# Optimization experiments

Measured on AMD Instinct MI355X. Metric: run time of the kernel, lower is better.

## Reference

```python
import jax, jax.numpy as jnp
import numpy as np

EPS = 1e-16


def setup_inputs() -> dict:
    key = jax.random.key(0)
    ks = jax.random.split(key, 8)
    B, C, F, H = 524288, 10, 10, 8  # batch, clusters, feats/cluster, tail hidden
    HC = 8  # head hidden = ceil(10 * 0.75)
    return {
        "x": jax.random.uniform(ks[0], (B, C * F), dtype=jnp.float32),
        "tail_enc_w": jax.random.normal(ks[1], (C, H, F), dtype=jnp.float32) * 0.3,
        "tail_enc_b": jax.random.normal(ks[2], (C, H), dtype=jnp.float32) * 0.1,
        "tail_dec_w": jax.random.normal(ks[3], (C, F, H), dtype=jnp.float32) * 0.3,
        "tail_dec_b": jax.random.normal(ks[4], (C, F), dtype=jnp.float32) * 0.1,
        "tail_nmin": jnp.zeros((C, F), dtype=jnp.float32),
        "tail_nmax": jnp.ones((C, F), dtype=jnp.float32),
        "head_enc_w": jax.random.normal(ks[5], (HC, C), dtype=jnp.float32) * 0.3,
        "head_enc_b": jax.random.normal(ks[6], (HC,), dtype=jnp.float32) * 0.1,
        "head_dec_w": jax.random.normal(ks[7], (C, HC), dtype=jnp.float32) * 0.3,
        "head_dec_b": jnp.zeros((C,), dtype=jnp.float32),
        "head_nmin": jnp.zeros((C,), dtype=jnp.float32),
        "head_nmax": jnp.ones((C,), dtype=jnp.float32),
    }


def reference(x, tail_enc_w, tail_enc_b, tail_dec_w, tail_dec_b,
              tail_nmin, tail_nmax, head_enc_w, head_enc_b,
              head_dec_w, head_dec_b, head_nmin, head_nmax):
    B = x.shape[0]
    C, H, F = tail_enc_w.shape
    # split the 100 features into C contiguous clusters of size F: [B, C, F]
    xc = x.reshape(B, C, F)
    # per-tail min-max normalisation (BaseAutoencoder.normalise)
    xn = (xc - tail_nmin) / (tail_nmax - tail_nmin + EPS)
    # all tails batched into one grouped matmul (sigmoid(Linear) twice)
    h = jax.nn.sigmoid(jnp.einsum('bcf,chf->bch', xn, tail_enc_w) + tail_enc_b)
    rec = jax.nn.sigmoid(jnp.einsum('bch,cfh->bcf', h, tail_dec_w) + tail_dec_b)
    # RMSE per (packet, cluster); infer mode => no log
    loss = jnp.sqrt(jnp.mean((rec - xn) ** 2, axis=-1))  # [B, C]
    tails = jnp.where(loss == 0, jnp.float32(0.01), loss)
    # head-level min-max normalisation (Kitsune.normalise)
    t = (tails - head_nmin) / (head_nmax - head_nmin + EPS)
    hh = jax.nn.sigmoid(t @ head_enc_w.T + head_enc_b)
    x_hat = jax.nn.sigmoid(hh @ head_dec_w.T + head_dec_b)
    return x_hat, t
```

## Files before the change

kernel.cpp:

```cpp
#include <hip/hip_runtime.h>

#define KEPS  1e-16f
#define LOG2E 1.44269504088896340736f

typedef float v2f __attribute__((ext_vector_type(2)));


__global__ void kitsune_prep(
    const float* __restrict__ tew, const float* __restrict__ teb,
    const float* __restrict__ tdw, const float* __restrict__ tdb,
    const float* __restrict__ tnmin, const float* __restrict__ tnmax,
    const float* __restrict__ hew, const float* __restrict__ heb,
    const float* __restrict__ hdw, const float* __restrict__ hdb,
    const float* __restrict__ hnmin, const float* __restrict__ hnmax,
    float* __restrict__ ws)
{
    const int i = threadIdx.x;
    for (int k = i; k < 100; k += 256) {
        float s = 1.0f / (tnmax[k] - tnmin[k] + KEPS);
        ws[k]        = s;
        ws[100 + k]  = -tnmin[k] * s;
        ws[1880 + k] = tdb[k] * -LOG2E;
    }
    for (int k = i; k < 800; k += 256) {
        ws[200 + k]  = tew[k] * -LOG2E;
        ws[1080 + k] = tdw[k] * -LOG2E;
    }
    for (int k = i; k < 80; k += 256) {
        ws[1000 + k] = teb[k] * -LOG2E;
        ws[2000 + k] = hew[k] * -LOG2E;
        ws[2088 + k] = hdw[k] * -LOG2E;
    }
    if (i < 10) {
        float s = 1.0f / (hnmax[i] - hnmin[i] + KEPS);
        ws[1980 + i] = s;
        ws[1990 + i] = -hnmin[i] * s;
        ws[2168 + i] = hdb[i] * -LOG2E;
    }
    if (i < 8) ws[2080 + i] = heb[i] * -LOG2E;
}

__device__ __forceinline__ float sig2(float a) {
    return __builtin_amdgcn_rcpf(1.0f + __builtin_amdgcn_exp2f(a));
}

__global__ __launch_bounds__(320) void kitsune_fused(
    const float* __restrict__ x,
    const float* __restrict__ ws,
    float* __restrict__ out_xhat,
    float* __restrict__ out_t,
    int B)
{
    __shared__ float xs[64 * 102];
    __shared__ float ts[64 * 11];

    const int tid  = threadIdx.x;
    const int base = (int)blockIdx.x * 64;
    const int rows = min(64, B - base);
    const int n25  = rows * 25;

    {
        const float4* gx = reinterpret_cast<const float4*>(x) + (size_t)base * 25;
        #pragma unroll
        for (int n = 0; n < 5; ++n) {
            int idx = tid + n * 320;
            if (idx < n25) {
                float4 v = gx[idx];
                int row = idx / 25;
                int q   = idx - row * 25;
                float* d = xs + row * 102 + q * 4;
                *reinterpret_cast<float2*>(d)     = make_float2(v.x, v.y);
                *reinterpret_cast<float2*>(d + 2) = make_float2(v.z, v.w);
            }
        }
    }
    __syncthreads();

    const int r = tid & 63;

    #pragma unroll
    for (int k = 0; k < 2; ++k) {
        const int c = __builtin_amdgcn_readfirstlane((tid >> 6) + 5 * k);

        v2f xp[5];
        #pragma unroll
        for (int j = 0; j < 5; ++j)
            xp[j] = *reinterpret_cast<const v2f*>(xs + r * 102 + c * 10 + 2 * j);

        const v2f* sc2 = reinterpret_cast<const v2f*>(ws + c * 10);
        const v2f* bi2 = reinterpret_cast<const v2f*>(ws + 100 + c * 10);
        #pragma unroll
        for (int j = 0; j < 5; ++j)
            xp[j] = __builtin_elementwise_fma(xp[j], sc2[j], bi2[j]);

        v2f hv[4];
        #pragma unroll
        for (int i = 0; i < 8; ++i) {
            const v2f* w2 = reinterpret_cast<const v2f*>(ws + 200 + (c * 8 + i) * 10);
            v2f a2 = w2[0] * xp[0];
            #pragma unroll
            for (int j = 1; j < 5; ++j)
                a2 = __builtin_elementwise_fma(w2[j], xp[j], a2);
            hv[i >> 1][i & 1] = sig2(ws[1000 + c * 8 + i] + a2.x + a2.y);
        }

        v2f ss2 = {0.0f, 0.0f};
        float dprev = 0.0f;
        #pragma unroll
        for (int f = 0; f < 10; ++f) {
            const v2f* w2 = reinterpret_cast<const v2f*>(ws + 1080 + (c * 10 + f) * 8);
            v2f a2 = w2[0] * hv[0];
            #pragma unroll
            for (int i = 1; i < 4; ++i)
                a2 = __builtin_elementwise_fma(w2[i], hv[i], a2);
            float rec = sig2(ws[1880 + c * 10 + f] + a2.x + a2.y);
            float d   = rec - xp[f >> 1][f & 1];
            if (f & 1) {
                v2f d2 = {dprev, d};
                ss2 = __builtin_elementwise_fma(d2, d2, ss2);
            } else {
                dprev = d;
            }
        }
        float l    = __builtin_amdgcn_sqrtf((ss2.x + ss2.y) * 0.1f);
        float tail = (l == 0.0f) ? 0.01f : l;
        float tv   = fmaf(tail, ws[1980 + c], ws[1990 + c]);

        ts[r * 11 + c] = tv;
        if (r < rows)
            out_t[(size_t)(base + r) * 10 + c] = tv;
    }
    __syncthreads();

    if (tid < 64 && tid < rows) {
        const float* tr = ts + tid * 11;
        v2f tp[5];
        #pragma unroll
        for (int j = 0; j < 5; ++j)
            tp[j] = v2f{tr[2 * j], tr[2 * j + 1]};

        v2f hv[4];
        #pragma unroll
        for (int i = 0; i < 8; ++i) {
            const v2f* w2 = reinterpret_cast<const v2f*>(ws + 2000 + i * 10);
            v2f a2 = w2[0] * tp[0];
            #pragma unroll
            for (int j = 1; j < 5; ++j)
                a2 = __builtin_elementwise_fma(w2[j], tp[j], a2);
            hv[i >> 1][i & 1] = sig2(ws[2080 + i] + a2.x + a2.y);
        }

        float xh[10];
        #pragma unroll
        for (int c = 0; c < 10; ++c) {
            const v2f* w2 = reinterpret_cast<const v2f*>(ws + 2088 + c * 8);
            v2f a2 = w2[0] * hv[0];
            #pragma unroll
            for (int i = 1; i < 4; ++i)
                a2 = __builtin_elementwise_fma(w2[i], hv[i], a2);
            xh[c] = sig2(ws[2168 + c] + a2.x + a2.y);
        }

        float* po = out_xhat + (size_t)(base + tid) * 10;
        #pragma unroll
        for (int j = 0; j < 5; ++j)
            *reinterpret_cast<float2*>(po + 2 * j) = make_float2(xh[2 * j], xh[2 * j + 1]);
    }
}

extern "C" void kernel_launch(void* const* d_in, const int* in_sizes, int n_in,
                              void* d_out, int out_size, void* d_ws, size_t ws_size,
                              hipStream_t stream) {
    const float* x          = (const float*)d_in[0];
    const float* tail_enc_w = (const float*)d_in[1];
    const float* tail_enc_b = (const float*)d_in[2];
    const float* tail_dec_w = (const float*)d_in[3];
    const float* tail_dec_b = (const float*)d_in[4];
    const float* tail_nmin  = (const float*)d_in[5];
    const float* tail_nmax  = (const float*)d_in[6];
    const float* head_enc_w = (const float*)d_in[7];
    const float* head_enc_b = (const float*)d_in[8];
    const float* head_dec_w = (const float*)d_in[9];
    const float* head_dec_b = (const float*)d_in[10];
    const float* head_nmin  = (const float*)d_in[11];
    const float* head_nmax  = (const float*)d_in[12];

    const int B = in_sizes[0] / 100;

    float* out_xhat = (float*)d_out;
    float* out_t    = out_xhat + (size_t)B * 10;
    float* ws       = (float*)d_ws;

    kitsune_prep<<<1, 256, 0, stream>>>(
        tail_enc_w, tail_enc_b, tail_dec_w, tail_dec_b, tail_nmin, tail_nmax,
        head_enc_w, head_enc_b, head_dec_w, head_dec_b, head_nmin, head_nmax, ws);

    const int grid = (B + 63) / 64;
    kitsune_fused<<<grid, 320, 0, stream>>>(x, ws, out_xhat, out_t, B);
}
```

Baseline: 68.58 us.

## Process two row tiles per block, prefetching the second tile into registers

Each block now handles 128 rows as two 64-row tiles. Global loads for the second tile are issued into registers before the first tile is computed, then committed to shared memory while the head stage of the first tile runs. The aim is to hide global load latency behind compute and halve the number of blocks. The cost is extra registers for the prefetched tile (which may lower occupancy), additional barriers, and fewer blocks in flight.

```diff
diff --git a/kernel.cpp b/kernel.cpp
--- a/kernel.cpp
+++ b/kernel.cpp
@@ -44,40 +44,26 @@
     return __builtin_amdgcn_rcpf(1.0f + __builtin_amdgcn_exp2f(a));
 }
 
-__global__ __launch_bounds__(320) void kitsune_fused(
-    const float* __restrict__ x,
-    const float* __restrict__ ws,
-    float* __restrict__ out_xhat,
-    float* __restrict__ out_t,
-    int B)
-{
-    __shared__ float xs[64 * 102];
-    __shared__ float ts[64 * 11];
-
-    const int tid  = threadIdx.x;
-    const int base = (int)blockIdx.x * 64;
-    const int rows = min(64, B - base);
-    const int n25  = rows * 25;
-
-    {
-        const float4* gx = reinterpret_cast<const float4*>(x) + (size_t)base * 25;
-        #pragma unroll
-        for (int n = 0; n < 5; ++n) {
-            int idx = tid + n * 320;
-            if (idx < n25) {
-                float4 v = gx[idx];
-                int row = idx / 25;
-                int q   = idx - row * 25;
-                float* d = xs + row * 102 + q * 4;
-                *reinterpret_cast<float2*>(d)     = make_float2(v.x, v.y);
-                *reinterpret_cast<float2*>(d + 2) = make_float2(v.z, v.w);
-            }
-        }
-    }
-    __syncthreads();
-
+__device__ __forceinline__ void commit_tile(float* xs, const float4* p,
+                                            int tid, int ncap) {
+    #pragma unroll
+    for (int n = 0; n < 5; ++n) {
+        int idx = tid + n * 320;
+        if (idx < ncap) {
+            int row = idx / 25;
+            int q   = idx - row * 25;
+            float* d = xs + row * 102 + q * 4;
+            *reinterpret_cast<float2*>(d)     = make_float2(p[n].x, p[n].y);
+            *reinterpret_cast<float2*>(d + 2) = make_float2(p[n].z, p[n].w);
+        }
+    }
+}
+
+__device__ __forceinline__ void tail_compute(const float* xs, float* ts,
+                                             const float* __restrict__ ws,
+                                             float* __restrict__ out_t,
+                                             int tid, int base, int rows) {
     const int r = tid & 63;
-
     #pragma unroll
     for (int k = 0; k < 2; ++k) {
         const int c = __builtin_amdgcn_readfirstlane((tid >> 6) + 5 * k);
@@ -130,8 +116,12 @@
         if (r < rows)
             out_t[(size_t)(base + r) * 10 + c] = tv;
     }
-    __syncthreads();
-
+}
+
+__device__ __forceinline__ void head_compute(const float* ts,
+                                             const float* __restrict__ ws,
+                                             float* __restrict__ out_xhat,
+                                             int tid, int base, int rows) {
     if (tid < 64 && tid < rows) {
         const float* tr = ts + tid * 11;
         v2f tp[5];
@@ -166,6 +156,61 @@
         for (int j = 0; j < 5; ++j)
             *reinterpret_cast<float2*>(po + 2 * j) = make_float2(xh[2 * j], xh[2 * j + 1]);
     }
+}
+
+__global__ __launch_bounds__(320) void kitsune_fused(
+    const float* __restrict__ x,
+    const float* __restrict__ ws,
+    float* __restrict__ out_xhat,
+    float* __restrict__ out_t,
+    int B)
+{
+    __shared__ float xs[64 * 102];
+    __shared__ float ts[64 * 11];
+
+    const int tid   = threadIdx.x;
+    const int base0 = (int)blockIdx.x * 128;
+    if (base0 >= B) return;
+    const int base1 = base0 + 64;
+    const int rows0 = min(64, B - base0);
+    const int n0    = rows0 * 25;
+    const int rows1 = (base1 < B) ? min(64, B - base1) : 0;
+    const int n1    = rows1 * 25;
+
+    const float4* gx = reinterpret_cast<const float4*>(x);
+
+    {
+        float4 p[5];
+        #pragma unroll
+        for (int n = 0; n < 5; ++n) {
+            int idx = tid + n * 320;
+            if (idx < n0) p[n] = gx[(size_t)base0 * 25 + idx];
+        }
+        commit_tile(xs, p, tid, n0);
+    }
+
+    float4 q[5];
+    if (rows1 > 0) {
+        #pragma unroll
+        for (int n = 0; n < 5; ++n) {
+            int idx = tid + n * 320;
+            if (idx < n1) q[n] = gx[(size_t)base1 * 25 + idx];
+        }
+    }
+    __syncthreads();
+
+    tail_compute(xs, ts, ws, out_t, tid, base0, rows0);
+    __syncthreads();
+
+    if (rows1 > 0) commit_tile(xs, q, tid, n1);
+    head_compute(ts, ws, out_xhat, tid, base0, rows0);
+    __syncthreads();
+
+    if (rows1 == 0) return;
+
+    tail_compute(xs, ts, ws, out_t, tid, base1, rows1);
+    __syncthreads();
+    head_compute(ts, ws, out_xhat, tid, base1, rows1);
 }
 
 extern "C" void kernel_launch(void* const* d_in, const int* in_sizes, int n_in,
@@ -195,6 +240,6 @@
         tail_enc_w, tail_enc_b, tail_dec_w, tail_dec_b, tail_nmin, tail_nmax,
         head_enc_w, head_enc_b, head_dec_w, head_dec_b, head_nmin, head_nmax, ws);
 
-    const int grid = (B + 63) / 64;
+    const int grid = (B + 127) / 128;
     kitsune_fused<<<grid, 320, 0, stream>>>(x, ws, out_xhat, out_t, B);
 }
```

New measurement: 68.32 us. Within noise of the previous version (-0.4%).
